# Optimization experiments

Measured on AMD Instinct MI355X. Metric: run time of the kernel, lower is better.

The kernel has to match this reference:

```python
import jax, jax.numpy as jnp
import numpy as np

B, P, E, D, A, M, V, L = 128, 196, 2048, 512, 512, 512, 10000, 21


def setup_inputs() -> dict:
    key = jax.random.key(0)
    ks = jax.random.split(key, 24)
    s = 0.02
    encoder_out = jax.random.normal(ks[0], (B, P, E), jnp.float32)
    encoded_captions = jax.random.randint(ks[1], (B, L), 0, V)
    caption_lengths = jax.random.randint(ks[2], (B,), 2, L + 1).at[0].set(L)
    return {
        "encoder_out": encoder_out,
        "encoded_captions": encoded_captions,
        "caption_lengths": caption_lengths,
        "emb_table": jax.random.normal(ks[3], (V, M), jnp.float32) * s,
        "enc_att_w": jax.random.normal(ks[4], (E, A), jnp.float32) * s,
        "enc_att_b": jnp.zeros((A,), jnp.float32),
        "dec_att_w": jax.random.normal(ks[5], (D, A), jnp.float32) * s,
        "dec_att_b": jnp.zeros((A,), jnp.float32),
        "full_att_w": jax.random.normal(ks[6], (A,), jnp.float32) * s,
        "full_att_b": jnp.zeros((), jnp.float32),
        "init_h_w": jax.random.normal(ks[7], (E, D), jnp.float32) * s,
        "init_h_b": jnp.zeros((D,), jnp.float32),
        "init_c_w": jax.random.normal(ks[8], (E, D), jnp.float32) * s,
        "init_c_b": jnp.zeros((D,), jnp.float32),
        "f_beta_w": jax.random.normal(ks[9], (D, E), jnp.float32) * s,
        "f_beta_b": jnp.zeros((E,), jnp.float32),
        "lstm_w_ih": jax.random.normal(ks[10], (4 * D, M + E), jnp.float32) * s,
        "lstm_b_ih": jnp.zeros((4 * D,), jnp.float32),
        "lstm_w_hh": jax.random.normal(ks[11], (4 * D, D), jnp.float32) * s,
        "lstm_b_hh": jnp.zeros((4 * D,), jnp.float32),
        "fc_w": jax.random.normal(ks[12], (V, D), jnp.float32) * s,
        "fc_b": jnp.zeros((V,), jnp.float32),
    }


def reference(encoder_out, encoded_captions, caption_lengths, emb_table,
              enc_att_w, enc_att_b, dec_att_w, dec_att_b, full_att_w, full_att_b,
              init_h_w, init_h_b, init_c_w, init_c_b, f_beta_w, f_beta_b,
              lstm_w_ih, lstm_b_ih, lstm_w_hh, lstm_b_hh, fc_w, fc_b):
    # sort by caption length descending (as in torch)
    order = jnp.argsort(-caption_lengths)
    enc = encoder_out[order]                 # [B,P,E]
    caps = encoded_captions[order]           # [B,L]
    dec_len = caption_lengths[order] - 1     # [B]
    T = caps.shape[1] - 1

    emb_seq = emb_table[caps]                # [B,L,M]
    mean = enc.mean(axis=1)                  # [B,E]
    h0 = mean @ init_h_w + init_h_b
    c0 = mean @ init_c_w + init_c_b
    att1 = enc @ enc_att_w + enc_att_b       # [B,P,A] (hoisted: constant over t)

    def step(carry, t):
        h, c = carry
        att2 = h @ dec_att_w + dec_att_b                              # [B,A]
        e = jnp.einsum('bpa,a->bp', jax.nn.relu(att1 + att2[:, None, :]), full_att_w) + full_att_b
        alpha = jax.nn.softmax(e, axis=1)                             # [B,P]
        awe = jnp.einsum('bpe,bp->be', enc, alpha)                    # [B,E]
        gate = jax.nn.sigmoid(h @ f_beta_w + f_beta_b)                # [B,E]
        x = jnp.concatenate([emb_seq[:, t, :], gate * awe], axis=1)   # [B,M+E]
        g = x @ lstm_w_ih.T + lstm_b_ih + h @ lstm_w_hh.T + lstm_b_hh
        i, f, gg, o = jnp.split(g, 4, axis=1)
        c_new = jax.nn.sigmoid(f) * c + jax.nn.sigmoid(i) * jnp.tanh(gg)
        h_new = jax.nn.sigmoid(o) * jnp.tanh(c_new)
        pred = h_new @ fc_w.T + fc_b                                  # [B,V]
        active = (t < dec_len)[:, None]
        pred = jnp.where(active, pred, 0.0)
        alpha = jnp.where(active, alpha, 0.0)
        return (h_new, c_new), (pred, alpha)

    _, (preds, alphas) = jax.lax.scan(step, (h0, c0), jnp.arange(T))
    predictions = jnp.moveaxis(preds, 0, 1)   # [B,T,V]
    alphas = jnp.moveaxis(alphas, 0, 1)       # [B,T,P]
    return predictions, alphas
```

## Files before the change

### kernel.cpp

```cpp
#include <hip/hip_runtime.h>
#include <math.h>

#define B_ 128
#define P_ 196
#define E_ 2048
#define D_ 512
#define A_ 512
#define M_ 512
#define V_ 10000
#define L_ 21
#define T_ 20

typedef __attribute__((ext_vector_type(8))) short bf16x8;
typedef __attribute__((ext_vector_type(4))) float f32x4;

__global__ void order_kernel(const int* __restrict__ lens, const int* __restrict__ caps,
                             int* __restrict__ order, int* __restrict__ declen,
                             int* __restrict__ row_map, int* __restrict__ tok_rows) {
  __shared__ int s_order[B_];
  int tid = threadIdx.x;
  if (tid < B_) {
    int li = lens[tid];
    int r = 0;
    for (int j = 0; j < B_; ++j) {
      int lj = lens[j];
      r += (lj > li) || (lj == li && j < tid);
    }
    s_order[r] = tid;
    declen[r] = li - 1;
  }
  __syncthreads();
  if (tid < B_) order[tid] = s_order[tid];
  for (int m = tid; m < B_ * P_; m += blockDim.x) {
    int b = m / P_, p = m - b * P_;
    row_map[m] = s_order[b] * P_ + p;
  }
  for (int i = tid; i < T_ * B_; i += blockDim.x) {
    int t = i >> 7, b = i & 127;
    tok_rows[i] = caps[s_order[b] * L_ + t];
  }
}

__global__ void mean_kernel(const float* __restrict__ enc, const int* __restrict__ order,
                            float* __restrict__ mean) {
  int b = blockIdx.y;
  int e = blockIdx.x * blockDim.x + threadIdx.x;
  int ob = order[b];
  const float* base = enc + (long long)ob * P_ * E_ + e;
  float s = 0.f;
  for (int p = 0; p < P_; ++p) s += base[(long long)p * E_];
  mean[b * E_ + e] = s * (1.0f / P_);
}

__global__ void transpose_kernel(const float* __restrict__ in, float* __restrict__ out) {
  __shared__ float t[32][33];
  int bx = blockIdx.x * 32;
  int by = blockIdx.y * 32;
  int lx = threadIdx.x & 31, ly = threadIdx.x >> 5;
#pragma unroll
  for (int i = 0; i < 32; i += 8) t[ly + i][lx] = in[(by + ly + i) * 512 + bx + lx];
  __syncthreads();
#pragma unroll
  for (int i = 0; i < 32; i += 8) out[(long long)(bx + ly + i) * 2048 + by + lx] = t[lx][ly + i];
}

__global__ __launch_bounds__(256) void gemm32_kernel(
    const float* __restrict__ A, const float* __restrict__ Bm,
    const float* __restrict__ bias, float* __restrict__ C,
    int M, int N, int K, float* __restrict__ xh_dup) {
  __shared__ float As[16][64];
  __shared__ float Bs[16][64];
  const int tid = threadIdx.x;
  const int bm = blockIdx.y * 64, bn = blockIdx.x * 64;
  const int tm = tid >> 4, tn = tid & 15;
  float acc[4][4];
#pragma unroll
  for (int i = 0; i < 4; ++i)
#pragma unroll
    for (int j = 0; j < 4; ++j) acc[i][j] = 0.f;
  const int lm = tid >> 2;
  const int lk = (tid & 3) * 4;
  for (int k0 = 0; k0 < K; k0 += 16) {
    {
      int m = bm + lm;
      float4 v = make_float4(0.f, 0.f, 0.f, 0.f);
      if (m < M) v = *(const float4*)(A + (long long)m * K + k0 + lk);
      As[lk + 0][lm] = v.x;
      As[lk + 1][lm] = v.y;
      As[lk + 2][lm] = v.z;
      As[lk + 3][lm] = v.w;
    }
    {
      int k = tid >> 4;
      int n4 = (tid & 15) * 4;
      int n = bn + n4;
      float4 v = make_float4(0.f, 0.f, 0.f, 0.f);
      if (n < N) v = *(const float4*)(Bm + (long long)(k0 + k) * N + n);
      Bs[k][n4 + 0] = v.x;
      Bs[k][n4 + 1] = v.y;
      Bs[k][n4 + 2] = v.z;
      Bs[k][n4 + 3] = v.w;
    }
    __syncthreads();
#pragma unroll
    for (int k = 0; k < 16; ++k) {
      float a0 = As[k][tm * 4 + 0], a1 = As[k][tm * 4 + 1];
      float a2 = As[k][tm * 4 + 2], a3 = As[k][tm * 4 + 3];
      float b0 = Bs[k][tn * 4 + 0], b1 = Bs[k][tn * 4 + 1];
      float b2 = Bs[k][tn * 4 + 2], b3 = Bs[k][tn * 4 + 3];
      acc[0][0] += a0 * b0; acc[0][1] += a0 * b1; acc[0][2] += a0 * b2; acc[0][3] += a0 * b3;
      acc[1][0] += a1 * b0; acc[1][1] += a1 * b1; acc[1][2] += a1 * b2; acc[1][3] += a1 * b3;
      acc[2][0] += a2 * b0; acc[2][1] += a2 * b1; acc[2][2] += a2 * b2; acc[2][3] += a2 * b3;
      acc[3][0] += a3 * b0; acc[3][1] += a3 * b1; acc[3][2] += a3 * b2; acc[3][3] += a3 * b3;
    }
    __syncthreads();
  }
#pragma unroll
  for (int i = 0; i < 4; ++i) {
    int m = bm + tm * 4 + i;
    if (m >= M) continue;
#pragma unroll
    for (int j = 0; j < 4; ++j) {
      int n = bn + tn * 4 + j;
      if (n >= N) continue;
      float v = acc[i][j] + (bias ? bias[n] : 0.f);
      C[(long long)m * N + n] = v;
      if (xh_dup) xh_dup[m * 2560 + 2048 + n] = v;
    }
  }
}

__device__ __forceinline__ unsigned f2bf_u(float f) {
  unsigned u = __float_as_uint(f);
  return (u + 0x7fffu + ((u >> 16) & 1u)) >> 16;
}

__device__ __forceinline__ void stage16(short* __restrict__ Ph, short* __restrict__ Pl,
                                        int r, int kq, float4 v0, float4 v1, float4 v2,
                                        float4 v3, bool split) {
  float f[16] = {v0.x, v0.y, v0.z, v0.w, v1.x, v1.y, v1.z, v1.w,
                 v2.x, v2.y, v2.z, v2.w, v3.x, v3.y, v3.z, v3.w};
#pragma unroll
  for (int g2 = 0; g2 < 2; ++g2) {
    int gg = (kq >> 3) + g2;
    int slot = gg ^ ((r >> 1) & 3);
    unsigned hb[8];
    float lf[8];
#pragma unroll
    for (int j = 0; j < 8; ++j) {
      float x = f[g2 * 8 + j];
      hb[j] = f2bf_u(x);
      lf[j] = x - __uint_as_float(hb[j] << 16);
    }
    int4 ph;
    ph.x = (int)(hb[0] | (hb[1] << 16));
    ph.y = (int)(hb[2] | (hb[3] << 16));
    ph.z = (int)(hb[4] | (hb[5] << 16));
    ph.w = (int)(hb[6] | (hb[7] << 16));
    *(int4*)&Ph[r * 32 + slot * 8] = ph;
    if (split) {
      unsigned lb[8];
#pragma unroll
      for (int j = 0; j < 8; ++j) lb[j] = f2bf_u(lf[j]);
      int4 pl;
      pl.x = (int)(lb[0] | (lb[1] << 16));
      pl.y = (int)(lb[2] | (lb[3] << 16));
      pl.z = (int)(lb[4] | (lb[5] << 16));
      pl.w = (int)(lb[6] | (lb[7] << 16));
      *(int4*)&Pl[r * 32 + slot * 8] = pl;
    }
  }
}

__device__ __forceinline__ bf16x8 frag_load(const short* __restrict__ P, int row, int g) {
  int slot = g ^ ((row >> 1) & 3);
  return *(const bf16x8*)&P[row * 32 + slot * 8];
}

template <int MODE, bool SPLIT>
__global__ __launch_bounds__(256) void mfma_gemm(
    const float* __restrict__ A, int lda, const int* __restrict__ row_map,
    const float* __restrict__ Bn, int ldb,
    const float* __restrict__ bias, const float* __restrict__ bias2,
    float* __restrict__ C, int ldc, int M, int N, int K,
    const float* __restrict__ whh, const int* __restrict__ declen) {
  __shared__ short Ah[128 * 32];
  __shared__ short Bh[128 * 32];
  __shared__ short Al[128 * 32];
  __shared__ short Bl[128 * 32];
  const int tid = threadIdx.x;
  int bm = blockIdx.y * 128, bn = blockIdx.x * 128;
  if (MODE == 2) {
    int z = blockIdx.z;
    A += z * 512;
    if (z < 4) {
      Bn += 512 + z * 512;
    } else {
      Bn = whh;
      ldb = 512;
    }
    C += (long long)z * (128 * 2048);
  }
  f32x4 acc[4][4];
#pragma unroll
  for (int i = 0; i < 4; ++i)
#pragma unroll
    for (int j = 0; j < 4; ++j) acc[i][j] = (f32x4){0.f, 0.f, 0.f, 0.f};

  const int r = tid >> 1;
  const int kq = (tid & 1) * 16;
  const int am = bm + r;
  const long long arow = row_map ? (long long)row_map[am] : (long long)am;
  const float* ap = A + arow * (long long)lda + kq;
  const int gn = bn + r;
  const float* bp = Bn + (long long)gn * ldb + kq;
  const bool bok = gn < N;

  const int lane = tid & 63;
  const int wv = tid >> 6, wr = wv >> 1, wc = wv & 1;
  const int lr = lane & 15, g = lane >> 4;

  for (int k0 = 0; k0 < K; k0 += 32) {
    float4 a0 = *(const float4*)(ap + k0);
    float4 a1 = *(const float4*)(ap + k0 + 4);
    float4 a2 = *(const float4*)(ap + k0 + 8);
    float4 a3 = *(const float4*)(ap + k0 + 12);
    float4 z4 = make_float4(0.f, 0.f, 0.f, 0.f);
    float4 b0 = bok ? *(const float4*)(bp + k0) : z4;
    float4 b1 = bok ? *(const float4*)(bp + k0 + 4) : z4;
    float4 b2 = bok ? *(const float4*)(bp + k0 + 8) : z4;
    float4 b3 = bok ? *(const float4*)(bp + k0 + 12) : z4;
    stage16(Ah, Al, r, kq, a0, a1, a2, a3, SPLIT);
    stage16(Bh, Bl, r, kq, b0, b1, b2, b3, SPLIT);
    __syncthreads();
    bf16x8 ah[4], bh[4];
#pragma unroll
    for (int i = 0; i < 4; ++i) {
      ah[i] = frag_load(Ah, wr * 64 + i * 16 + lr, g);
      bh[i] = frag_load(Bh, wc * 64 + i * 16 + lr, g);
    }
#pragma unroll
    for (int i = 0; i < 4; ++i)
#pragma unroll
      for (int j = 0; j < 4; ++j)
        acc[i][j] = __builtin_amdgcn_mfma_f32_16x16x32_bf16(ah[i], bh[j], acc[i][j], 0, 0, 0);
    if (SPLIT) {
      bf16x8 al2[4], bl2[4];
#pragma unroll
      for (int i = 0; i < 4; ++i) {
        al2[i] = frag_load(Al, wr * 64 + i * 16 + lr, g);
        bl2[i] = frag_load(Bl, wc * 64 + i * 16 + lr, g);
      }
#pragma unroll
      for (int i = 0; i < 4; ++i)
#pragma unroll
        for (int j = 0; j < 4; ++j)
          acc[i][j] = __builtin_amdgcn_mfma_f32_16x16x32_bf16(al2[i], bh[j], acc[i][j], 0, 0, 0);
#pragma unroll
      for (int i = 0; i < 4; ++i)
#pragma unroll
        for (int j = 0; j < 4; ++j)
          acc[i][j] = __builtin_amdgcn_mfma_f32_16x16x32_bf16(ah[i], bl2[j], acc[i][j], 0, 0, 0);
    }
    __syncthreads();
  }

#pragma unroll
  for (int j = 0; j < 4; ++j) {
    int n = bn + wc * 64 + j * 16 + lr;
    float bj = 0.f;
    if (n < N) {
      if (bias) bj += bias[n];
      if (bias2) bj += bias2[n];
    }
#pragma unroll
    for (int i = 0; i < 4; ++i) {
#pragma unroll
      for (int rr = 0; rr < 4; ++rr) {
        int m = bm + wr * 64 + i * 16 + g * 4 + rr;
        float v = acc[i][j][rr] + bj;
        if (MODE == 0) {
          C[(long long)m * ldc + n] = v;
        } else if (MODE == 1) {
          if (n < N) {
            int b = m & 127, t = m >> 7;
            C[(long long)b * (T_ * V_) + (long long)t * V_ + n] = (t < declen[b]) ? v : 0.f;
          }
        } else {
          C[(long long)m * ldc + n] = v;
        }
      }
    }
  }
}

__global__ __launch_bounds__(256) void step1_kernel(
    const float* __restrict__ h, const float* __restrict__ dec_att_w,
    const float* __restrict__ dec_att_b, const float* __restrict__ f_beta_w,
    const float* __restrict__ f_beta_b, float* __restrict__ att2,
    float* __restrict__ gate) {
  __shared__ float As[16][64];
  __shared__ float Bs[16][64];
  const int tid = threadIdx.x;
  const int bm = blockIdx.y * 64, bn = blockIdx.x * 64;
  const bool isatt = bn < 512;
  const float* Bp = isatt ? dec_att_w : f_beta_w;
  const int bstride = isatt ? 512 : 2048;
  const int ncol0 = isatt ? bn : bn - 512;
  const int tm = tid >> 4, tn = tid & 15;
  float acc[4][4];
#pragma unroll
  for (int i = 0; i < 4; ++i)
#pragma unroll
    for (int j = 0; j < 4; ++j) acc[i][j] = 0.f;
  const int lm = tid >> 2;
  const int lk = (tid & 3) * 4;
  for (int k0 = 0; k0 < 512; k0 += 16) {
    {
      int m = bm + lm;
      float4 v = *(const float4*)(h + m * 512 + k0 + lk);
      As[lk + 0][lm] = v.x;
      As[lk + 1][lm] = v.y;
      As[lk + 2][lm] = v.z;
      As[lk + 3][lm] = v.w;
    }
    {
      int k = tid >> 4;
      int n4 = (tid & 15) * 4;
      float4 v = *(const float4*)(Bp + (k0 + k) * bstride + ncol0 + n4);
      Bs[k][n4 + 0] = v.x;
      Bs[k][n4 + 1] = v.y;
      Bs[k][n4 + 2] = v.z;
      Bs[k][n4 + 3] = v.w;
    }
    __syncthreads();
#pragma unroll
    for (int k = 0; k < 16; ++k) {
      float a0 = As[k][tm * 4 + 0], a1 = As[k][tm * 4 + 1];
      float a2 = As[k][tm * 4 + 2], a3 = As[k][tm * 4 + 3];
      float b0 = Bs[k][tn * 4 + 0], b1 = Bs[k][tn * 4 + 1];
      float b2 = Bs[k][tn * 4 + 2], b3 = Bs[k][tn * 4 + 3];
      acc[0][0] += a0 * b0; acc[0][1] += a0 * b1; acc[0][2] += a0 * b2; acc[0][3] += a0 * b3;
      acc[1][0] += a1 * b0; acc[1][1] += a1 * b1; acc[1][2] += a1 * b2; acc[1][3] += a1 * b3;
      acc[2][0] += a2 * b0; acc[2][1] += a2 * b1; acc[2][2] += a2 * b2; acc[2][3] += a2 * b3;
      acc[3][0] += a3 * b0; acc[3][1] += a3 * b1; acc[3][2] += a3 * b2; acc[3][3] += a3 * b3;
    }
    __syncthreads();
  }
#pragma unroll
  for (int i = 0; i < 4; ++i) {
    int m = bm + tm * 4 + i;
#pragma unroll
    for (int j = 0; j < 4; ++j) {
      int nc = ncol0 + tn * 4 + j;
      float v = acc[i][j];
      if (isatt) {
        att2[m * 512 + nc] = v + dec_att_b[nc];
      } else {
        v += f_beta_b[nc];
        gate[m * 2048 + nc] = 1.f / (1.f + __expf(-v));
      }
    }
  }
}

__global__ __launch_bounds__(256) void esm_kernel(
    const float* __restrict__ att1, const float* __restrict__ att2,
    const float* __restrict__ w, const float* __restrict__ fb,
    const int* __restrict__ declen, int t,
    float* __restrict__ alpha_ws, float* __restrict__ alpha_out) {
  __shared__ float att2_s[A_];
  __shared__ float w_s[A_];
  __shared__ float e_s[P_];
  __shared__ float red[8];
  int b = blockIdx.x, tid = threadIdx.x;
  for (int i = tid; i < A_; i += 256) {
    att2_s[i] = att2[b * A_ + i];
    w_s[i] = w[i];
  }
  __syncthreads();
  int wave = tid >> 6, lane = tid & 63;
  for (int p = wave; p < P_; p += 4) {
    const float* row = att1 + ((long long)b * P_ + p) * A_;
    float s = 0.f;
#pragma unroll
    for (int i = 0; i < A_ / 64; ++i) {
      int idx = lane + i * 64;
      float v = row[idx] + att2_s[idx];
      s += (v > 0.f ? v : 0.f) * w_s[idx];
    }
    for (int off = 32; off; off >>= 1) s += __shfl_down(s, off);
    if (lane == 0) e_s[p] = s + fb[0];
  }
  __syncthreads();
  float m = -1e30f;
  for (int p = tid; p < P_; p += 256) m = fmaxf(m, e_s[p]);
  for (int off = 32; off; off >>= 1) m = fmaxf(m, __shfl_down(m, off));
  if (lane == 0) red[wave] = m;
  __syncthreads();
  m = fmaxf(fmaxf(red[0], red[1]), fmaxf(red[2], red[3]));
  float ssum = 0.f;
  for (int p = tid; p < P_; p += 256) {
    float ev = __expf(e_s[p] - m);
    e_s[p] = ev;
    ssum += ev;
  }
  for (int off = 32; off; off >>= 1) ssum += __shfl_down(ssum, off);
  if (lane == 0) red[4 + wave] = ssum;
  __syncthreads();
  ssum = red[4] + red[5] + red[6] + red[7];
  float inv = 1.f / ssum;
  bool active = (t < declen[b]);
  for (int p = tid; p < P_; p += 256) {
    float al = e_s[p] * inv;
    alpha_ws[b * P_ + p] = al;
    alpha_out[(long long)b * (T_ * P_) + t * P_ + p] = active ? al : 0.f;
  }
}

__global__ __launch_bounds__(256) void awe_kernel(
    const float* __restrict__ alpha_ws, const float* __restrict__ enc,
    const int* __restrict__ order, const float* __restrict__ gate,
    float* __restrict__ xh) {
  __shared__ float al[P_];
  int b = blockIdx.y;
  int e = blockIdx.x * 256 + threadIdx.x;
  for (int i = threadIdx.x; i < P_; i += 256) al[i] = alpha_ws[b * P_ + i];
  __syncthreads();
  int ob = order[b];
  const float* eb = enc + (long long)ob * P_ * E_ + e;
  float s = 0.f;
#pragma unroll 4
  for (int p = 0; p < P_; ++p) s += al[p] * eb[(long long)p * E_];
  xh[b * 2560 + e] = gate[b * 2048 + e] * s;
}

__global__ void lstm_ew_kernel(const float* __restrict__ g_emb,
                               const float* __restrict__ g_part,
                               float* __restrict__ c, float* __restrict__ h_next,
                               float* __restrict__ xh) {
  int idx = blockIdx.x * blockDim.x + threadIdx.x;
  int b = idx >> 9, d = idx & 511;
  int base = b * 2048 + d;
  float gi = g_emb[base], gf = g_emb[base + 512], gg = g_emb[base + 1024],
        go = g_emb[base + 1536];
#pragma unroll
  for (int z = 0; z < 5; ++z) {
    const float* gp = g_part + z * (128 * 2048) + base;
    gi += gp[0];
    gf += gp[512];
    gg += gp[1024];
    go += gp[1536];
  }
  float si = 1.f / (1.f + __expf(-gi));
  float sf = 1.f / (1.f + __expf(-gf));
  float so = 1.f / (1.f + __expf(-go));
  float cn = sf * c[idx] + si * tanhf(gg);
  float hn = so * tanhf(cn);
  c[idx] = cn;
  h_next[idx] = hn;
  xh[b * 2560 + 2048 + d] = hn;
}

extern "C" void kernel_launch(void* const* d_in, const int* in_sizes, int n_in,
                              void* d_out, int out_size, void* d_ws, size_t ws_size,
                              hipStream_t stream) {
  const float* enc       = (const float*)d_in[0];
  const int*   caps      = (const int*)d_in[1];
  const int*   lens      = (const int*)d_in[2];
  const float* emb       = (const float*)d_in[3];
  const float* enc_att_w = (const float*)d_in[4];
  const float* enc_att_b = (const float*)d_in[5];
  const float* dec_att_w = (const float*)d_in[6];
  const float* dec_att_b = (const float*)d_in[7];
  const float* full_att_w = (const float*)d_in[8];
  const float* full_att_b = (const float*)d_in[9];
  const float* init_h_w  = (const float*)d_in[10];
  const float* init_h_b  = (const float*)d_in[11];
  const float* init_c_w  = (const float*)d_in[12];
  const float* init_c_b  = (const float*)d_in[13];
  const float* f_beta_w  = (const float*)d_in[14];
  const float* f_beta_b  = (const float*)d_in[15];
  const float* lstm_w_ih = (const float*)d_in[16];
  const float* lstm_b_ih = (const float*)d_in[17];
  const float* lstm_w_hh = (const float*)d_in[18];
  const float* lstm_b_hh = (const float*)d_in[19];
  const float* fc_w      = (const float*)d_in[20];
  const float* fc_b      = (const float*)d_in[21];

  float* out = (float*)d_out;
  float* alphas_out = out + (long long)B_ * T_ * V_;

  float* g_all    = out;
  float* g_part   = out + 6 * 1024 * 1024;
  float* encattwT = out + 8 * 1024 * 1024;

  float* ws = (float*)d_ws;
  float* att1  = ws;
  float* mean  = att1 + (long long)B_ * P_ * A_;
  float* h_all = mean + B_ * E_;
  float* c     = h_all + (T_ + 1) * B_ * D_;
  float* att2  = c + B_ * D_;
  float* gate  = att2 + B_ * A_;
  float* xh    = gate + B_ * E_;
  float* alpha_ws = xh + B_ * (M_ + E_);
  int* order   = (int*)(alpha_ws + B_ * P_);
  int* declen  = order + B_;
  int* row_map = declen + B_;
  int* tok_rows = row_map + B_ * P_;

  hipLaunchKernelGGL(order_kernel, dim3(1), dim3(256), 0, stream, lens, caps, order, declen,
                     row_map, tok_rows);
  hipLaunchKernelGGL(mean_kernel, dim3(E_ / 256, B_), dim3(256), 0, stream, enc, order, mean);
  hipLaunchKernelGGL(transpose_kernel, dim3(16, 64), dim3(256), 0, stream, enc_att_w, encattwT);
  hipLaunchKernelGGL(gemm32_kernel, dim3(D_ / 64, 2), dim3(256), 0, stream, mean, init_h_w,
                     init_h_b, h_all, B_, D_, E_, xh);
  hipLaunchKernelGGL(gemm32_kernel, dim3(D_ / 64, 2), dim3(256), 0, stream, mean, init_c_w,
                     init_c_b, c, B_, D_, E_, (float*)nullptr);
  hipLaunchKernelGGL((mfma_gemm<0, false>), dim3(A_ / 128, (B_ * P_) / 128), dim3(256), 0,
                     stream, enc, E_, row_map, encattwT, E_, enc_att_b, (const float*)nullptr,
                     att1, A_, B_ * P_, A_, E_, (const float*)nullptr, (const int*)nullptr);
  hipLaunchKernelGGL((mfma_gemm<0, true>), dim3((4 * D_) / 128, (T_ * B_) / 128), dim3(256), 0,
                     stream, emb, M_, tok_rows, lstm_w_ih, M_ + E_, lstm_b_ih, lstm_b_hh,
                     g_all, 4 * D_, T_ * B_, 4 * D_, M_, (const float*)nullptr,
                     (const int*)nullptr);

  for (int t = 0; t < T_; ++t) {
    float* h_cur = h_all + (long long)t * B_ * D_;
    float* h_next = h_cur + B_ * D_;
    hipLaunchKernelGGL(step1_kernel, dim3(40, 2), dim3(256), 0, stream, h_cur, dec_att_w,
                       dec_att_b, f_beta_w, f_beta_b, att2, gate);
    hipLaunchKernelGGL(esm_kernel, dim3(B_), dim3(256), 0, stream, att1, att2, full_att_w,
                       full_att_b, declen, t, alpha_ws, alphas_out);
    hipLaunchKernelGGL(awe_kernel, dim3(E_ / 256, B_), dim3(256), 0, stream, alpha_ws, enc,
                       order, gate, xh);
    hipLaunchKernelGGL((mfma_gemm<2, true>), dim3((4 * D_) / 128, 1, 5), dim3(256), 0, stream,
                       xh, M_ + E_, (const int*)nullptr, lstm_w_ih, M_ + E_,
                       (const float*)nullptr, (const float*)nullptr, g_part, 4 * D_, B_,
                       4 * D_, D_, lstm_w_hh, (const int*)nullptr);
    hipLaunchKernelGGL(lstm_ew_kernel, dim3((B_ * D_) / 256), dim3(256), 0, stream,
                       g_all + (long long)t * B_ * (4 * D_), g_part, c, h_next, xh);
  }

  hipLaunchKernelGGL((mfma_gemm<1, true>), dim3((V_ + 127) / 128, (T_ * B_) / 128), dim3(256),
                     0, stream, h_all + B_ * D_, D_, (const int*)nullptr, fc_w, D_, fc_b,
                     (const float*)nullptr, out, V_, T_ * B_, V_, D_, (const float*)nullptr,
                     declen);
}
```

Baseline: 4.805 ms.

## Fuse per-timestep decoder kernels into one persistent kernel with grid barriers

Replaces the 100 per-step launches (step1, esm, awe, gate GEMM, lstm elementwise) with a single persistent 256-block kernel. It walks all timesteps and separates phases with atomic grid-wide barriers. The h-projections (att2, gate, W_hh) now run as one combined 64x64 MFMA tile phase, and the xh GEMM is split over K into 4 partial sums. It also adds register prefetch of the next K-slice in mfma_gemm and a grouped block swizzle for the att1 GEMM. The aim is to remove launch overhead and small-kernel tail effects. In exchange, the grid barrier relies on all 256 blocks being co-resident, and spin-waiting adds latency at each phase.

```diff
diff --git a/kernel.cpp b/kernel.cpp
--- a/kernel.cpp
+++ b/kernel.cpp
@@ -16,9 +16,11 @@
 
 __global__ void order_kernel(const int* __restrict__ lens, const int* __restrict__ caps,
                              int* __restrict__ order, int* __restrict__ declen,
-                             int* __restrict__ row_map, int* __restrict__ tok_rows) {
+                             int* __restrict__ row_map, int* __restrict__ tok_rows,
+                             unsigned* __restrict__ bar) {
   __shared__ int s_order[B_];
   int tid = threadIdx.x;
+  if (tid < 2) bar[tid] = 0u;
   if (tid < B_) {
     int li = lens[tid];
     int r = 0;
@@ -52,22 +54,23 @@
   mean[b * E_ + e] = s * (1.0f / P_);
 }
 
-__global__ void transpose_kernel(const float* __restrict__ in, float* __restrict__ out) {
-  __shared__ float t[32][33];
+__global__ void transpose_kernel(const float* __restrict__ in, float* __restrict__ out,
+                                 int K, int N) {
+  __shared__ float tt[32][33];
   int bx = blockIdx.x * 32;
   int by = blockIdx.y * 32;
   int lx = threadIdx.x & 31, ly = threadIdx.x >> 5;
 #pragma unroll
-  for (int i = 0; i < 32; i += 8) t[ly + i][lx] = in[(by + ly + i) * 512 + bx + lx];
+  for (int i = 0; i < 32; i += 8) tt[ly + i][lx] = in[(long long)(by + ly + i) * N + bx + lx];
   __syncthreads();
 #pragma unroll
-  for (int i = 0; i < 32; i += 8) out[(long long)(bx + ly + i) * 2048 + by + lx] = t[lx][ly + i];
+  for (int i = 0; i < 32; i += 8)
+    out[(long long)(bx + ly + i) * K + by + lx] = tt[lx][ly + i];
 }
 
 __global__ __launch_bounds__(256) void gemm32_kernel(
     const float* __restrict__ A, const float* __restrict__ Bm,
-    const float* __restrict__ bias, float* __restrict__ C,
-    int M, int N, int K, float* __restrict__ xh_dup) {
+    const float* __restrict__ bias, float* __restrict__ C, int M, int N, int K) {
   __shared__ float As[16][64];
   __shared__ float Bs[16][64];
   const int tid = threadIdx.x;
@@ -123,9 +126,7 @@
     for (int j = 0; j < 4; ++j) {
       int n = bn + tn * 4 + j;
       if (n >= N) continue;
-      float v = acc[i][j] + (bias ? bias[n] : 0.f);
-      C[(long long)m * N + n] = v;
-      if (xh_dup) xh_dup[m * 2560 + 2048 + n] = v;
+      C[(long long)m * N + n] = acc[i][j] + (bias ? bias[n] : 0.f);
     }
   }
 }
@@ -172,35 +173,72 @@
   }
 }
 
+__device__ __forceinline__ void stage8(short* __restrict__ Ph, short* __restrict__ Pl,
+                                       int r, int kq8, float4 v0, float4 v1) {
+  int slot = kq8 ^ ((r >> 1) & 3);
+  float f[8] = {v0.x, v0.y, v0.z, v0.w, v1.x, v1.y, v1.z, v1.w};
+  unsigned hb[8];
+  float lf[8];
+#pragma unroll
+  for (int j = 0; j < 8; ++j) {
+    hb[j] = f2bf_u(f[j]);
+    lf[j] = f[j] - __uint_as_float(hb[j] << 16);
+  }
+  int4 ph;
+  ph.x = (int)(hb[0] | (hb[1] << 16));
+  ph.y = (int)(hb[2] | (hb[3] << 16));
+  ph.z = (int)(hb[4] | (hb[5] << 16));
+  ph.w = (int)(hb[6] | (hb[7] << 16));
+  *(int4*)&Ph[r * 32 + slot * 8] = ph;
+  unsigned lb[8];
+#pragma unroll
+  for (int j = 0; j < 8; ++j) lb[j] = f2bf_u(lf[j]);
+  int4 pl;
+  pl.x = (int)(lb[0] | (lb[1] << 16));
+  pl.y = (int)(lb[2] | (lb[3] << 16));
+  pl.z = (int)(lb[4] | (lb[5] << 16));
+  pl.w = (int)(lb[6] | (lb[7] << 16));
+  *(int4*)&Pl[r * 32 + slot * 8] = pl;
+}
+
 __device__ __forceinline__ bf16x8 frag_load(const short* __restrict__ P, int row, int g) {
   int slot = g ^ ((row >> 1) & 3);
   return *(const bf16x8*)&P[row * 32 + slot * 8];
 }
 
-template <int MODE, bool SPLIT>
+template <int MODE, bool SPLIT, bool SWZ>
 __global__ __launch_bounds__(256) void mfma_gemm(
     const float* __restrict__ A, int lda, const int* __restrict__ row_map,
     const float* __restrict__ Bn, int ldb,
     const float* __restrict__ bias, const float* __restrict__ bias2,
     float* __restrict__ C, int ldc, int M, int N, int K,
-    const float* __restrict__ whh, const int* __restrict__ declen) {
+    const int* __restrict__ declen) {
   __shared__ short Ah[128 * 32];
   __shared__ short Bh[128 * 32];
   __shared__ short Al[128 * 32];
   __shared__ short Bl[128 * 32];
   const int tid = threadIdx.x;
-  int bm = blockIdx.y * 128, bn = blockIdx.x * 128;
-  if (MODE == 2) {
-    int z = blockIdx.z;
-    A += z * 512;
-    if (z < 4) {
-      Bn += 512 + z * 512;
+  int bxi, byi;
+  if (SWZ) {
+    int gx = gridDim.x, gy = gridDim.y;
+    int id = blockIdx.y * gx + blockIdx.x;
+    int super = 8 * gx;
+    int body = (gy & ~7) * gx;
+    if (id < body) {
+      int s = id / super, rem = id % super;
+      byi = s * 8 + (rem & 7);
+      bxi = rem >> 3;
     } else {
-      Bn = whh;
-      ldb = 512;
-    }
-    C += (long long)z * (128 * 2048);
-  }
+      int rem = id - body;
+      byi = (gy & ~7) + rem / gx;
+      bxi = rem % gx;
+    }
+  } else {
+    bxi = blockIdx.x;
+    byi = blockIdx.y;
+  }
+  const int bm = byi * 128, bn = bxi * 128;
+
   f32x4 acc[4][4];
 #pragma unroll
   for (int i = 0; i < 4; ++i)
@@ -220,19 +258,29 @@
   const int wv = tid >> 6, wr = wv >> 1, wc = wv & 1;
   const int lr = lane & 15, g = lane >> 4;
 
+  float4 z4 = make_float4(0.f, 0.f, 0.f, 0.f);
+  float4 a0 = *(const float4*)(ap), a1 = *(const float4*)(ap + 4);
+  float4 a2 = *(const float4*)(ap + 8), a3 = *(const float4*)(ap + 12);
+  float4 b0 = bok ? *(const float4*)(bp) : z4;
+  float4 b1 = bok ? *(const float4*)(bp + 4) : z4;
+  float4 b2 = bok ? *(const float4*)(bp + 8) : z4;
+  float4 b3 = bok ? *(const float4*)(bp + 12) : z4;
+
   for (int k0 = 0; k0 < K; k0 += 32) {
-    float4 a0 = *(const float4*)(ap + k0);
-    float4 a1 = *(const float4*)(ap + k0 + 4);
-    float4 a2 = *(const float4*)(ap + k0 + 8);
-    float4 a3 = *(const float4*)(ap + k0 + 12);
-    float4 z4 = make_float4(0.f, 0.f, 0.f, 0.f);
-    float4 b0 = bok ? *(const float4*)(bp + k0) : z4;
-    float4 b1 = bok ? *(const float4*)(bp + k0 + 4) : z4;
-    float4 b2 = bok ? *(const float4*)(bp + k0 + 8) : z4;
-    float4 b3 = bok ? *(const float4*)(bp + k0 + 12) : z4;
     stage16(Ah, Al, r, kq, a0, a1, a2, a3, SPLIT);
     stage16(Bh, Bl, r, kq, b0, b1, b2, b3, SPLIT);
     __syncthreads();
+    if (k0 + 32 < K) {
+      int kn = k0 + 32;
+      a0 = *(const float4*)(ap + kn);
+      a1 = *(const float4*)(ap + kn + 4);
+      a2 = *(const float4*)(ap + kn + 8);
+      a3 = *(const float4*)(ap + kn + 12);
+      b0 = bok ? *(const float4*)(bp + kn) : z4;
+      b1 = bok ? *(const float4*)(bp + kn + 4) : z4;
+      b2 = bok ? *(const float4*)(bp + kn + 8) : z4;
+      b3 = bok ? *(const float4*)(bp + kn + 12) : z4;
+    }
     bf16x8 ah[4], bh[4];
 #pragma unroll
     for (int i = 0; i < 4; ++i) {
@@ -281,185 +329,247 @@
         float v = acc[i][j][rr] + bj;
         if (MODE == 0) {
           C[(long long)m * ldc + n] = v;
-        } else if (MODE == 1) {
+        } else {
           if (n < N) {
             int b = m & 127, t = m >> 7;
             C[(long long)b * (T_ * V_) + (long long)t * V_ + n] = (t < declen[b]) ? v : 0.f;
           }
-        } else {
-          C[(long long)m * ldc + n] = v;
         }
       }
     }
   }
 }
 
-__global__ __launch_bounds__(256) void step1_kernel(
-    const float* __restrict__ h, const float* __restrict__ dec_att_w,
-    const float* __restrict__ dec_att_b, const float* __restrict__ f_beta_w,
-    const float* __restrict__ f_beta_b, float* __restrict__ att2,
-    float* __restrict__ gate) {
-  __shared__ float As[16][64];
-  __shared__ float Bs[16][64];
-  const int tid = threadIdx.x;
-  const int bm = blockIdx.y * 64, bn = blockIdx.x * 64;
-  const bool isatt = bn < 512;
-  const float* Bp = isatt ? dec_att_w : f_beta_w;
-  const int bstride = isatt ? 512 : 2048;
-  const int ncol0 = isatt ? bn : bn - 512;
-  const int tm = tid >> 4, tn = tid & 15;
-  float acc[4][4];
-#pragma unroll
-  for (int i = 0; i < 4; ++i)
-#pragma unroll
-    for (int j = 0; j < 4; ++j) acc[i][j] = 0.f;
-  const int lm = tid >> 2;
-  const int lk = (tid & 3) * 4;
-  for (int k0 = 0; k0 < 512; k0 += 16) {
-    {
-      int m = bm + lm;
-      float4 v = *(const float4*)(h + m * 512 + k0 + lk);
-      As[lk + 0][lm] = v.x;
-      As[lk + 1][lm] = v.y;
-      As[lk + 2][lm] = v.z;
-      As[lk + 3][lm] = v.w;
-    }
-    {
-      int k = tid >> 4;
-      int n4 = (tid & 15) * 4;
-      float4 v = *(const float4*)(Bp + (k0 + k) * bstride + ncol0 + n4);
-      Bs[k][n4 + 0] = v.x;
-      Bs[k][n4 + 1] = v.y;
-      Bs[k][n4 + 2] = v.z;
-      Bs[k][n4 + 3] = v.w;
-    }
+__device__ __forceinline__ void mfma_tile64(
+    const float* __restrict__ ap, const float* __restrict__ bp, int K,
+    f32x4 (&acc)[2][2], short* Ah, short* Al, short* Bh, short* Bl,
+    int sr, int skq, int wr, int wc, int lr, int g) {
+  float4 a0 = *(const float4*)(ap), a1 = *(const float4*)(ap + 4);
+  float4 b0 = *(const float4*)(bp), b1 = *(const float4*)(bp + 4);
+  for (int k0 = 0; k0 < K; k0 += 32) {
+    stage8(Ah, Al, sr, skq, a0, a1);
+    stage8(Bh, Bl, sr, skq, b0, b1);
     __syncthreads();
-#pragma unroll
-    for (int k = 0; k < 16; ++k) {
-      float a0 = As[k][tm * 4 + 0], a1 = As[k][tm * 4 + 1];
-      float a2 = As[k][tm * 4 + 2], a3 = As[k][tm * 4 + 3];
-      float b0 = Bs[k][tn * 4 + 0], b1 = Bs[k][tn * 4 + 1];
-      float b2 = Bs[k][tn * 4 + 2], b3 = Bs[k][tn * 4 + 3];
-      acc[0][0] += a0 * b0; acc[0][1] += a0 * b1; acc[0][2] += a0 * b2; acc[0][3] += a0 * b3;
-      acc[1][0] += a1 * b0; acc[1][1] += a1 * b1; acc[1][2] += a1 * b2; acc[1][3] += a1 * b3;
-      acc[2][0] += a2 * b0; acc[2][1] += a2 * b1; acc[2][2] += a2 * b2; acc[2][3] += a2 * b3;
-      acc[3][0] += a3 * b0; acc[3][1] += a3 * b1; acc[3][2] += a3 * b2; acc[3][3] += a3 * b3;
-    }
+    if (k0 + 32 < K) {
+      a0 = *(const float4*)(ap + k0 + 32);
+      a1 = *(const float4*)(ap + k0 + 36);
+      b0 = *(const float4*)(bp + k0 + 32);
+      b1 = *(const float4*)(bp + k0 + 36);
+    }
+    bf16x8 fah[2], fbh[2], fal[2], fbl[2];
+#pragma unroll
+    for (int i = 0; i < 2; ++i) {
+      fah[i] = frag_load(Ah, wr * 32 + i * 16 + lr, g);
+      fal[i] = frag_load(Al, wr * 32 + i * 16 + lr, g);
+      fbh[i] = frag_load(Bh, wc * 32 + i * 16 + lr, g);
+      fbl[i] = frag_load(Bl, wc * 32 + i * 16 + lr, g);
+    }
+#pragma unroll
+    for (int i = 0; i < 2; ++i)
+#pragma unroll
+      for (int j = 0; j < 2; ++j) {
+        acc[i][j] = __builtin_amdgcn_mfma_f32_16x16x32_bf16(fah[i], fbh[j], acc[i][j], 0, 0, 0);
+        acc[i][j] = __builtin_amdgcn_mfma_f32_16x16x32_bf16(fal[i], fbh[j], acc[i][j], 0, 0, 0);
+        acc[i][j] = __builtin_amdgcn_mfma_f32_16x16x32_bf16(fah[i], fbl[j], acc[i][j], 0, 0, 0);
+      }
     __syncthreads();
   }
-#pragma unroll
-  for (int i = 0; i < 4; ++i) {
-    int m = bm + tm * 4 + i;
-#pragma unroll
-    for (int j = 0; j < 4; ++j) {
-      int nc = ncol0 + tn * 4 + j;
-      float v = acc[i][j];
-      if (isatt) {
-        att2[m * 512 + nc] = v + dec_att_b[nc];
-      } else {
-        v += f_beta_b[nc];
-        gate[m * 2048 + nc] = 1.f / (1.f + __expf(-v));
-      }
-    }
-  }
-}
-
-__global__ __launch_bounds__(256) void esm_kernel(
-    const float* __restrict__ att1, const float* __restrict__ att2,
-    const float* __restrict__ w, const float* __restrict__ fb,
-    const int* __restrict__ declen, int t,
-    float* __restrict__ alpha_ws, float* __restrict__ alpha_out) {
-  __shared__ float att2_s[A_];
-  __shared__ float w_s[A_];
+}
+
+__device__ __forceinline__ void gsync(unsigned* cnt, unsigned* flag, unsigned nblk,
+                                      unsigned target) {
+  __syncthreads();
+  if (threadIdx.x == 0) {
+    __threadfence();
+    unsigned old = __hip_atomic_fetch_add(cnt, 1u, __ATOMIC_ACQ_REL,
+                                          __HIP_MEMORY_SCOPE_AGENT);
+    if (old == nblk - 1u) {
+      __hip_atomic_store(cnt, 0u, __ATOMIC_RELAXED, __HIP_MEMORY_SCOPE_AGENT);
+      __hip_atomic_store(flag, target, __ATOMIC_RELEASE, __HIP_MEMORY_SCOPE_AGENT);
+    } else {
+      while (__hip_atomic_load(flag, __ATOMIC_ACQUIRE, __HIP_MEMORY_SCOPE_AGENT) < target) {
+        __builtin_amdgcn_s_sleep(2);
+      }
+    }
+    __threadfence();
+  }
+  __syncthreads();
+}
+
+__global__ __launch_bounds__(256, 1) void loop_kernel(
+    const float* __restrict__ att1, const float* __restrict__ enc,
+    const int* __restrict__ order, const int* __restrict__ declen,
+    const float* __restrict__ decT, const float* __restrict__ decb,
+    const float* __restrict__ fbT, const float* __restrict__ fbb,
+    const float* __restrict__ whh, const float* __restrict__ wih,
+    const float* __restrict__ faw, const float* __restrict__ fab,
+    const float* __restrict__ g_all, float* __restrict__ g_part,
+    float* __restrict__ gh, float* __restrict__ h_all, float* __restrict__ c,
+    float* __restrict__ xh, float* __restrict__ gate, float* __restrict__ att2,
+    float* __restrict__ alphas_out, unsigned* __restrict__ bar) {
+  __shared__ short Ah[64 * 32];
+  __shared__ short Bh[64 * 32];
+  __shared__ short Al[64 * 32];
+  __shared__ short Bl[64 * 32];
+  __shared__ float att2_s[512];
+  __shared__ float w_s[512];
   __shared__ float e_s[P_];
   __shared__ float red[8];
-  int b = blockIdx.x, tid = threadIdx.x;
-  for (int i = tid; i < A_; i += 256) {
-    att2_s[i] = att2[b * A_ + i];
-    w_s[i] = w[i];
-  }
-  __syncthreads();
-  int wave = tid >> 6, lane = tid & 63;
-  for (int p = wave; p < P_; p += 4) {
-    const float* row = att1 + ((long long)b * P_ + p) * A_;
-    float s = 0.f;
-#pragma unroll
-    for (int i = 0; i < A_ / 64; ++i) {
-      int idx = lane + i * 64;
-      float v = row[idx] + att2_s[idx];
-      s += (v > 0.f ? v : 0.f) * w_s[idx];
-    }
-    for (int off = 32; off; off >>= 1) s += __shfl_down(s, off);
-    if (lane == 0) e_s[p] = s + fb[0];
-  }
-  __syncthreads();
-  float m = -1e30f;
-  for (int p = tid; p < P_; p += 256) m = fmaxf(m, e_s[p]);
-  for (int off = 32; off; off >>= 1) m = fmaxf(m, __shfl_down(m, off));
-  if (lane == 0) red[wave] = m;
-  __syncthreads();
-  m = fmaxf(fmaxf(red[0], red[1]), fmaxf(red[2], red[3]));
-  float ssum = 0.f;
-  for (int p = tid; p < P_; p += 256) {
-    float ev = __expf(e_s[p] - m);
-    e_s[p] = ev;
-    ssum += ev;
-  }
-  for (int off = 32; off; off >>= 1) ssum += __shfl_down(ssum, off);
-  if (lane == 0) red[4 + wave] = ssum;
-  __syncthreads();
-  ssum = red[4] + red[5] + red[6] + red[7];
-  float inv = 1.f / ssum;
-  bool active = (t < declen[b]);
-  for (int p = tid; p < P_; p += 256) {
-    float al = e_s[p] * inv;
-    alpha_ws[b * P_ + p] = al;
-    alpha_out[(long long)b * (T_ * P_) + t * P_ + p] = active ? al : 0.f;
-  }
-}
-
-__global__ __launch_bounds__(256) void awe_kernel(
-    const float* __restrict__ alpha_ws, const float* __restrict__ enc,
-    const int* __restrict__ order, const float* __restrict__ gate,
-    float* __restrict__ xh) {
-  __shared__ float al[P_];
-  int b = blockIdx.y;
-  int e = blockIdx.x * 256 + threadIdx.x;
-  for (int i = threadIdx.x; i < P_; i += 256) al[i] = alpha_ws[b * P_ + i];
-  __syncthreads();
-  int ob = order[b];
-  const float* eb = enc + (long long)ob * P_ * E_ + e;
-  float s = 0.f;
+
+  unsigned* cnt = bar;
+  unsigned* flag = bar + 1;
+  unsigned tgt = 0;
+
+  const int bid = blockIdx.x, tid = threadIdx.x;
+  const int lane = tid & 63, wv = tid >> 6, wr = wv >> 1, wc = wv & 1;
+  const int lr = lane & 15, g = lane >> 4;
+  const int sr = tid >> 2, skq = tid & 3;
+
+  for (int t = 0; t < T_; ++t) {
+    const float* h_cur = h_all + t * (B_ * D_);
+    if (bid < 144) {
+      int nt = bid % 72, mt = bid / 72;
+      int bn = nt * 64;
+      const float* Bb;
+      if (bn < 512) Bb = decT + bn * 512;
+      else if (bn < 2560) Bb = fbT + (bn - 512) * 512;
+      else Bb = whh + (bn - 2560) * 512;
+      f32x4 acc[2][2];
+#pragma unroll
+      for (int i = 0; i < 2; ++i)
+#pragma unroll
+        for (int j = 0; j < 2; ++j) acc[i][j] = (f32x4){0.f, 0.f, 0.f, 0.f};
+      mfma_tile64(h_cur + (mt * 64 + sr) * 512 + skq * 8, Bb + sr * 512 + skq * 8, 512,
+                  acc, Ah, Al, Bh, Bl, sr, skq, wr, wc, lr, g);
+#pragma unroll
+      for (int j = 0; j < 2; ++j) {
+        int n = bn + wc * 32 + j * 16 + lr;
+#pragma unroll
+        for (int i = 0; i < 2; ++i) {
+#pragma unroll
+          for (int rr = 0; rr < 4; ++rr) {
+            int m = mt * 64 + wr * 32 + i * 16 + g * 4 + rr;
+            float v = acc[i][j][rr];
+            if (bn < 512) {
+              att2[m * 512 + n] = v + decb[n];
+            } else if (bn < 2560) {
+              int nc = n - 512;
+              gate[m * 2048 + nc] = 1.f / (1.f + __expf(-(v + fbb[nc])));
+            } else {
+              gh[m * 2048 + (n - 2560)] = v;
+            }
+          }
+        }
+      }
+    }
+    gsync(cnt, flag, 256, ++tgt);
+    {
+      const int b = bid & 127, half = bid >> 7;
+      for (int i = tid; i < 512; i += 256) {
+        att2_s[i] = att2[b * 512 + i];
+        w_s[i] = faw[i];
+      }
+      __syncthreads();
+      for (int p = wv; p < P_; p += 4) {
+        const float* row = att1 + ((long long)b * P_ + p) * 512;
+        float s = 0.f;
+#pragma unroll
+        for (int i2 = 0; i2 < 8; ++i2) {
+          int ix = lane + i2 * 64;
+          float v = row[ix] + att2_s[ix];
+          s += (v > 0.f ? v : 0.f) * w_s[ix];
+        }
+        for (int off = 32; off; off >>= 1) s += __shfl_down(s, off);
+        if (lane == 0) e_s[p] = s + fab[0];
+      }
+      __syncthreads();
+      float mx = -1e30f;
+      for (int p = tid; p < P_; p += 256) mx = fmaxf(mx, e_s[p]);
+      for (int off = 32; off; off >>= 1) mx = fmaxf(mx, __shfl_down(mx, off));
+      if (lane == 0) red[wv] = mx;
+      __syncthreads();
+      mx = fmaxf(fmaxf(red[0], red[1]), fmaxf(red[2], red[3]));
+      float ssum = 0.f;
+      for (int p = tid; p < P_; p += 256) {
+        float ev = __expf(e_s[p] - mx);
+        e_s[p] = ev;
+        ssum += ev;
+      }
+      for (int off = 32; off; off >>= 1) ssum += __shfl_down(ssum, off);
+      if (lane == 0) red[4 + wv] = ssum;
+      __syncthreads();
+      float inv = 1.f / (red[4] + red[5] + red[6] + red[7]);
+      const bool active = (t < declen[b]);
+      for (int p = tid; p < P_; p += 256) {
+        float al = e_s[p] * inv;
+        e_s[p] = al;
+        if (half == 0)
+          alphas_out[(long long)b * (T_ * P_) + t * P_ + p] = active ? al : 0.f;
+      }
+      __syncthreads();
+      const int ob = order[b];
+      const float* eb = enc + (long long)ob * (P_ * E_);
+      for (int e0 = half * 1024 + tid; e0 < half * 1024 + 1024; e0 += 256) {
+        float s2 = 0.f;
 #pragma unroll 4
-  for (int p = 0; p < P_; ++p) s += al[p] * eb[(long long)p * E_];
-  xh[b * 2560 + e] = gate[b * 2048 + e] * s;
-}
-
-__global__ void lstm_ew_kernel(const float* __restrict__ g_emb,
-                               const float* __restrict__ g_part,
-                               float* __restrict__ c, float* __restrict__ h_next,
-                               float* __restrict__ xh) {
-  int idx = blockIdx.x * blockDim.x + threadIdx.x;
-  int b = idx >> 9, d = idx & 511;
-  int base = b * 2048 + d;
-  float gi = g_emb[base], gf = g_emb[base + 512], gg = g_emb[base + 1024],
-        go = g_emb[base + 1536];
-#pragma unroll
-  for (int z = 0; z < 5; ++z) {
-    const float* gp = g_part + z * (128 * 2048) + base;
-    gi += gp[0];
-    gf += gp[512];
-    gg += gp[1024];
-    go += gp[1536];
-  }
-  float si = 1.f / (1.f + __expf(-gi));
-  float sf = 1.f / (1.f + __expf(-gf));
-  float so = 1.f / (1.f + __expf(-go));
-  float cn = sf * c[idx] + si * tanhf(gg);
-  float hn = so * tanhf(cn);
-  c[idx] = cn;
-  h_next[idx] = hn;
-  xh[b * 2560 + 2048 + d] = hn;
+        for (int p = 0; p < P_; ++p) s2 += e_s[p] * eb[p * 2048 + e0];
+        xh[b * 2048 + e0] = gate[b * 2048 + e0] * s2;
+      }
+    }
+    gsync(cnt, flag, 256, ++tgt);
+    {
+      int kc = bid >> 6, rem = bid & 63, mt = rem >> 5, nt = rem & 31;
+      int bn = nt * 64;
+      f32x4 acc[2][2];
+#pragma unroll
+      for (int i = 0; i < 2; ++i)
+#pragma unroll
+        for (int j = 0; j < 2; ++j) acc[i][j] = (f32x4){0.f, 0.f, 0.f, 0.f};
+      mfma_tile64(xh + (mt * 64 + sr) * 2048 + kc * 512 + skq * 8,
+                  wih + (long long)(bn + sr) * 2560 + 512 + kc * 512 + skq * 8, 512,
+                  acc, Ah, Al, Bh, Bl, sr, skq, wr, wc, lr, g);
+      float* gp = g_part + kc * (128 * 2048);
+#pragma unroll
+      for (int j = 0; j < 2; ++j) {
+        int n = bn + wc * 32 + j * 16 + lr;
+#pragma unroll
+        for (int i = 0; i < 2; ++i) {
+#pragma unroll
+          for (int rr = 0; rr < 4; ++rr) {
+            int m = mt * 64 + wr * 32 + i * 16 + g * 4 + rr;
+            gp[m * 2048 + n] = acc[i][j][rr];
+          }
+        }
+      }
+    }
+    gsync(cnt, flag, 256, ++tgt);
+    {
+      int idx = bid * 256 + tid;
+      int b = idx >> 9, d = idx & 511;
+      int base = b * 2048 + d;
+      const float* ge = g_all + (long long)t * (128 * 2048);
+      float gi = ge[base] + gh[base];
+      float gf2 = ge[base + 512] + gh[base + 512];
+      float gg2 = ge[base + 1024] + gh[base + 1024];
+      float go = ge[base + 1536] + gh[base + 1536];
+#pragma unroll
+      for (int kc = 0; kc < 4; ++kc) {
+        const float* gp = g_part + kc * (128 * 2048) + base;
+        gi += gp[0];
+        gf2 += gp[512];
+        gg2 += gp[1024];
+        go += gp[1536];
+      }
+      float si = 1.f / (1.f + __expf(-gi));
+      float sf = 1.f / (1.f + __expf(-gf2));
+      float so = 1.f / (1.f + __expf(-go));
+      float cn = sf * c[idx] + si * tanhf(gg2);
+      float hn = so * tanhf(cn);
+      c[idx] = cn;
+      h_all[(t + 1) * (B_ * D_) + idx] = hn;
+    }
+    gsync(cnt, flag, 256, ++tgt);
+  }
 }
 
 extern "C" void kernel_launch(void* const* d_in, const int* in_sizes, int n_in,
@@ -494,6 +604,9 @@
   float* g_all    = out;
   float* g_part   = out + 6 * 1024 * 1024;
   float* encattwT = out + 8 * 1024 * 1024;
+  float* decT     = out + 9 * 1024 * 1024 + 512 * 1024;
+  float* fbT      = decT + 512 * 512;
+  float* gh       = out + 12 * 1024 * 1024;
 
   float* ws = (float*)d_ws;
   float* att1  = ws;
@@ -503,47 +616,36 @@
   float* att2  = c + B_ * D_;
   float* gate  = att2 + B_ * A_;
   float* xh    = gate + B_ * E_;
-  float* alpha_ws = xh + B_ * (M_ + E_);
-  int* order   = (int*)(alpha_ws + B_ * P_);
+  int* order   = (int*)(xh + B_ * E_);
   int* declen  = order + B_;
   int* row_map = declen + B_;
   int* tok_rows = row_map + B_ * P_;
+  unsigned* bar = (unsigned*)(tok_rows + T_ * B_);
 
   hipLaunchKernelGGL(order_kernel, dim3(1), dim3(256), 0, stream, lens, caps, order, declen,
-                     row_map, tok_rows);
+                     row_map, tok_rows, bar);
+  hipLaunchKernelGGL(transpose_kernel, dim3(16, 64), dim3(256), 0, stream, enc_att_w,
+                     encattwT, E_, A_);
+  hipLaunchKernelGGL(transpose_kernel, dim3(16, 16), dim3(256), 0, stream, dec_att_w, decT,
+                     D_, A_);
+  hipLaunchKernelGGL(transpose_kernel, dim3(64, 16), dim3(256), 0, stream, f_beta_w, fbT,
+                     D_, E_);
   hipLaunchKernelGGL(mean_kernel, dim3(E_ / 256, B_), dim3(256), 0, stream, enc, order, mean);
-  hipLaunchKernelGGL(transpose_kernel, dim3(16, 64), dim3(256), 0, stream, enc_att_w, encattwT);
   hipLaunchKernelGGL(gemm32_kernel, dim3(D_ / 64, 2), dim3(256), 0, stream, mean, init_h_w,
-                     init_h_b, h_all, B_, D_, E_, xh);
+                     init_h_b, h_all, B_, D_, E_);
   hipLaunchKernelGGL(gemm32_kernel, dim3(D_ / 64, 2), dim3(256), 0, stream, mean, init_c_w,
-                     init_c_b, c, B_, D_, E_, (float*)nullptr);
-  hipLaunchKernelGGL((mfma_gemm<0, false>), dim3(A_ / 128, (B_ * P_) / 128), dim3(256), 0,
-                     stream, enc, E_, row_map, encattwT, E_, enc_att_b, (const float*)nullptr,
-                     att1, A_, B_ * P_, A_, E_, (const float*)nullptr, (const int*)nullptr);
-  hipLaunchKernelGGL((mfma_gemm<0, true>), dim3((4 * D_) / 128, (T_ * B_) / 128), dim3(256), 0,
-                     stream, emb, M_, tok_rows, lstm_w_ih, M_ + E_, lstm_b_ih, lstm_b_hh,
-                     g_all, 4 * D_, T_ * B_, 4 * D_, M_, (const float*)nullptr,
-                     (const int*)nullptr);
-
-  for (int t = 0; t < T_; ++t) {
-    float* h_cur = h_all + (long long)t * B_ * D_;
-    float* h_next = h_cur + B_ * D_;
-    hipLaunchKernelGGL(step1_kernel, dim3(40, 2), dim3(256), 0, stream, h_cur, dec_att_w,
-                       dec_att_b, f_beta_w, f_beta_b, att2, gate);
-    hipLaunchKernelGGL(esm_kernel, dim3(B_), dim3(256), 0, stream, att1, att2, full_att_w,
-                       full_att_b, declen, t, alpha_ws, alphas_out);
-    hipLaunchKernelGGL(awe_kernel, dim3(E_ / 256, B_), dim3(256), 0, stream, alpha_ws, enc,
-                       order, gate, xh);
-    hipLaunchKernelGGL((mfma_gemm<2, true>), dim3((4 * D_) / 128, 1, 5), dim3(256), 0, stream,
-                       xh, M_ + E_, (const int*)nullptr, lstm_w_ih, M_ + E_,
-                       (const float*)nullptr, (const float*)nullptr, g_part, 4 * D_, B_,
-                       4 * D_, D_, lstm_w_hh, (const int*)nullptr);
-    hipLaunchKernelGGL(lstm_ew_kernel, dim3((B_ * D_) / 256), dim3(256), 0, stream,
-                       g_all + (long long)t * B_ * (4 * D_), g_part, c, h_next, xh);
-  }
-
-  hipLaunchKernelGGL((mfma_gemm<1, true>), dim3((V_ + 127) / 128, (T_ * B_) / 128), dim3(256),
-                     0, stream, h_all + B_ * D_, D_, (const int*)nullptr, fc_w, D_, fc_b,
-                     (const float*)nullptr, out, V_, T_ * B_, V_, D_, (const float*)nullptr,
-                     declen);
-}
+                     init_c_b, c, B_, D_, E_);
+  hipLaunchKernelGGL((mfma_gemm<0, false, true>), dim3(A_ / 128, (B_ * P_) / 128), dim3(256),
+                     0, stream, enc, E_, row_map, encattwT, E_, enc_att_b,
+                     (const float*)nullptr, att1, A_, B_ * P_, A_, E_, (const int*)nullptr);
+  hipLaunchKernelGGL((mfma_gemm<0, true, false>), dim3((4 * D_) / 128, (T_ * B_) / 128),
+                     dim3(256), 0, stream, emb, M_, tok_rows, lstm_w_ih, M_ + E_, lstm_b_ih,
+                     lstm_b_hh, g_all, 4 * D_, T_ * B_, 4 * D_, M_, (const int*)nullptr);
+  hipLaunchKernelGGL(loop_kernel, dim3(256), dim3(256), 0, stream, att1, enc, order, declen,
+                     decT, dec_att_b, fbT, f_beta_b, lstm_w_hh, lstm_w_ih, full_att_w,
+                     full_att_b, g_all, g_part, gh, h_all, c, xh, gate, att2, alphas_out,
+                     bar);
+  hipLaunchKernelGGL((mfma_gemm<1, true, false>), dim3((V_ + 127) / 128, (T_ * B_) / 128),
+                     dim3(256), 0, stream, h_all + B_ * D_, D_, (const int*)nullptr, fc_w, D_,
+                     fc_b, (const float*)nullptr, out, V_, T_ * B_, V_, D_, declen);
+}
```

Measured after the change: 8.025 ms. 67.0% more time.
